# Performance work log

Hardware: AMD Instinct MI355X
Metric: run time of the kernel (lower is better)

## Reference

```python
import jax, jax.numpy as jnp
import numpy as np


def setup_inputs() -> dict:
    key = jax.random.key(0)
    k1, k2 = jax.random.split(key)
    B, C, H, W = 2, 32, 128, 256
    left = jax.random.normal(k1, (B, C, H, W), dtype=jnp.float32)
    right = jax.random.normal(k2, (B, C, H, W), dtype=jnp.float32)
    return {"left": left, "right": right, "max_disp": 32}


def reference(left, right, max_disp):
    # left, right: [B, C, H, W] -> cost volume [B, 2C, D, H, W]
    B, C, H, W = left.shape
    d = jnp.arange(max_disp)          # [D]
    w = jnp.arange(W)                 # [W]
    # left slice for disparity d: left[..., w+d], zero where w+d >= W
    pos_l = w[None, :] + d[:, None]   # [D, W]
    mask_l = pos_l < W
    # right slice for disparity d: right[..., w-d], zero where w < d
    pos_r = w[None, :] - d[:, None]   # [D, W]
    mask_r = pos_r >= 0
    # gather along W: [B, C, H, D, W]
    lg = jnp.take(left, jnp.clip(pos_l, 0, W - 1), axis=-1)
    rg = jnp.take(right, jnp.clip(pos_r, 0, W - 1), axis=-1)
    lg = jnp.where(mask_l, lg, jnp.zeros((), left.dtype))
    rg = jnp.where(mask_r, rg, jnp.zeros((), right.dtype))
    # -> [B, C, D, H, W]
    lg = lg.transpose(0, 1, 3, 2, 4)
    rg = rg.transpose(0, 1, 3, 2, 4)
    return jnp.concatenate([lg, rg], axis=1)  # [B, 2C, D, H, W]
```

## Files before the change

### kernel.cpp

```cpp
#include <hip/hip_runtime.h>


__global__ __launch_bounds__(256) void costvol_kernel(
        const float* __restrict__ left,
        const float* __restrict__ right,
        float* __restrict__ out) {
    constexpr int W = 256, H = 128, D = 32, C = 32;
    (void)H; (void)D;

    unsigned n = blockIdx.x * 256u + threadIdx.x;
    unsigned w  = (n & 63u) << 2;
    unsigned r  = n >> 6;
    unsigned h  = r & 127u; r >>= 7;
    unsigned d  = r & 31u;  r >>= 5;
    unsigned c2 = r & 63u;  r >>= 6;
    unsigned b  = r;

    float4 v;
    if (c2 < C) {
        const float* row = left + (size_t)(((b * C + c2) * (unsigned)H + h)) * W;
        int base = (int)(w + d);
        v.x = (base + 0 < W) ? row[base + 0] : 0.f;
        v.y = (base + 1 < W) ? row[base + 1] : 0.f;
        v.z = (base + 2 < W) ? row[base + 2] : 0.f;
        v.w = (base + 3 < W) ? row[base + 3] : 0.f;
    } else {
        const float* row = right + (size_t)(((b * C + (c2 - C)) * (unsigned)H + h)) * W;
        int base = (int)w - (int)d;
        v.x = (base + 0 >= 0) ? row[base + 0] : 0.f;
        v.y = (base + 1 >= 0) ? row[base + 1] : 0.f;
        v.z = (base + 2 >= 0) ? row[base + 2] : 0.f;
        v.w = (base + 3 >= 0) ? row[base + 3] : 0.f;
    }
    reinterpret_cast<float4*>(out)[n] = v;
}

extern "C" void kernel_launch(void* const* d_in, const int* in_sizes, int n_in,
                              void* d_out, int out_size, void* d_ws, size_t ws_size,
                              hipStream_t stream) {
    const float* left  = (const float*)d_in[0];
    const float* right = (const float*)d_in[1];
    float* out = (float*)d_out;

    const unsigned n4 = (unsigned)(out_size / 4);
    const unsigned blocks = (n4 + 255u) / 256u;
    costvol_kernel<<<blocks, 256, 0, stream>>>(left, right, out);
}
```

Before: 614.1 us.

## Load each input row segment once into registers and emit all disparities

Each thread now loads a 36-float window of the left and right rows into registers with vector loads, then writes all 32 disparity outputs for both halves from those registers. This replaces one thread per output float4 that each issued four scalar, possibly unaligned loads. The grid shrinks to a fixed 2048 blocks, each thread doing 64 stores. Input traffic and index arithmetic drop, at the cost of higher register use, fewer threads and hardcoded shapes.

Result: faster. 540.4 us (-12.0%).

```diff
diff --git a/kernel.cpp b/kernel.cpp
--- a/kernel.cpp
+++ b/kernel.cpp
@@ -1,38 +1,57 @@
 #include <hip/hip_runtime.h>
 
+
+typedef float vfloat4 __attribute__((ext_vector_type(4)));
 
 __global__ __launch_bounds__(256) void costvol_kernel(
         const float* __restrict__ left,
         const float* __restrict__ right,
         float* __restrict__ out) {
-    constexpr int W = 256, H = 128, D = 32, C = 32;
-    (void)H; (void)D;
+    constexpr int W4 = 64, H = 128, D = 32, C = 32;
 
-    unsigned n = blockIdx.x * 256u + threadIdx.x;
-    unsigned w  = (n & 63u) << 2;
-    unsigned r  = n >> 6;
-    unsigned h  = r & 127u; r >>= 7;
-    unsigned d  = r & 31u;  r >>= 5;
-    unsigned c2 = r & 63u;  r >>= 6;
-    unsigned b  = r;
+    const unsigned tid = threadIdx.x;
+    const unsigned w4  = tid & 63u;
+    const unsigned hlo = tid >> 6;
+    const unsigned bid = blockIdx.x;
+    const unsigned h   = (bid & 31u) * 4u + hlo;
+    const unsigned c   = (bid >> 5) & 31u;
+    const unsigned b   = bid >> 10;
 
-    float4 v;
-    if (c2 < C) {
-        const float* row = left + (size_t)(((b * C + c2) * (unsigned)H + h)) * W;
-        int base = (int)(w + d);
-        v.x = (base + 0 < W) ? row[base + 0] : 0.f;
-        v.y = (base + 1 < W) ? row[base + 1] : 0.f;
-        v.z = (base + 2 < W) ? row[base + 2] : 0.f;
-        v.w = (base + 3 < W) ? row[base + 3] : 0.f;
-    } else {
-        const float* row = right + (size_t)(((b * C + (c2 - C)) * (unsigned)H + h)) * W;
-        int base = (int)w - (int)d;
-        v.x = (base + 0 >= 0) ? row[base + 0] : 0.f;
-        v.y = (base + 1 >= 0) ? row[base + 1] : 0.f;
-        v.z = (base + 2 >= 0) ? row[base + 2] : 0.f;
-        v.w = (base + 3 >= 0) ? row[base + 3] : 0.f;
+    const size_t inoff = ((size_t)(b * C + c) * H + h) * 256;
+    const vfloat4* lrow = reinterpret_cast<const vfloat4*>(left  + inoff);
+    const vfloat4* rrow = reinterpret_cast<const vfloat4*>(right + inoff);
+
+    const size_t dstride = (size_t)W4 * H;
+    vfloat4* outL = reinterpret_cast<vfloat4*>(out)
+                  + (size_t)w4
+                  + (size_t)W4 * ((size_t)h + (size_t)H * D * ((size_t)c + 2u * C * (size_t)b));
+    vfloat4* outR = outL + (size_t)C * D * dstride;
+
+    const vfloat4 zero4 = {0.f, 0.f, 0.f, 0.f};
+
+    float l[36];
+#pragma unroll
+    for (int k = 0; k < 9; ++k) {
+        vfloat4 v = (w4 + (unsigned)k < (unsigned)W4) ? lrow[w4 + k] : zero4;
+        l[4*k+0] = v.x; l[4*k+1] = v.y; l[4*k+2] = v.z; l[4*k+3] = v.w;
     }
-    reinterpret_cast<float4*>(out)[n] = v;
+#pragma unroll
+    for (int d = 0; d < D; ++d) {
+        vfloat4 q = { l[d], l[d+1], l[d+2], l[d+3] };
+        outL[(size_t)d * dstride] = q;
+    }
+
+    float r[36];
+#pragma unroll
+    for (int m = 0; m < 9; ++m) {
+        vfloat4 v = (w4 + (unsigned)m >= 8u) ? rrow[(int)(w4 + m) - 8] : zero4;
+        r[4*m+0] = v.x; r[4*m+1] = v.y; r[4*m+2] = v.z; r[4*m+3] = v.w;
+    }
+#pragma unroll
+    for (int d = 0; d < D; ++d) {
+        vfloat4 q = { r[32-d], r[33-d], r[34-d], r[35-d] };
+        outR[(size_t)d * dstride] = q;
+    }
 }
 
 extern "C" void kernel_launch(void* const* d_in, const int* in_sizes, int n_in,
@@ -42,7 +61,5 @@
     const float* right = (const float*)d_in[1];
     float* out = (float*)d_out;
 
-    const unsigned n4 = (unsigned)(out_size / 4);
-    const unsigned blocks = (n4 + 255u) / 256u;
-    costvol_kernel<<<blocks, 256, 0, stream>>>(left, right, out);
+    costvol_kernel<<<2048, 256, 0, stream>>>(left, right, out);
 }
```
